# Optimization experiments

Hardware: AMD Instinct MI355X
Metric: run time of the kernel (lower is better)

## Reference

```python
import jax, jax.numpy as jnp
import numpy as np

B, S, H, F, E, N, K = 2, 4096, 1024, 3584, 8, 2, 2


def setup_inputs() -> dict:
    key = jax.random.key(0)
    ks = jax.random.split(key, 6)
    scale_h = 1.0 / np.sqrt(H)
    scale_f = 1.0 / np.sqrt(F)
    return {
        "hidden_states": jax.random.normal(ks[0], (B, S, H), dtype=jnp.float32),
        "gate_w": jax.random.normal(ks[1], (E, H), dtype=jnp.float32) * scale_h,
        "gate2_w": jax.random.normal(ks[2], (N, H), dtype=jnp.float32) * scale_h,
        "w1": jax.random.normal(ks[3], (E, F, H), dtype=jnp.float32) * scale_h,
        "w2": jax.random.normal(ks[4], (E, H, F), dtype=jnp.float32) * scale_f,
        "w3": jax.random.normal(ks[5], (E, F, H), dtype=jnp.float32) * scale_h,
    }


def reference(hidden_states, gate_w, gate2_w, w1, w2, w3):
    b, s, h = hidden_states.shape
    x = hidden_states.reshape(-1, h)  # [T, H]

    # Router: real gate + null-expert gate, concatenated
    router_logits = jnp.concatenate([x @ gate_w.T, x @ gate2_w.T], axis=1)  # [T, E+N]
    rw = jax.nn.softmax(router_logits.astype(jnp.float32), axis=1)
    top_w, sel = jax.lax.top_k(rw, K)  # [T, K]

    # Null experts (idx >= E) get their raw weight; real experts are renormalized
    mask = sel < E
    sw = top_w * mask
    denom = sw.sum(axis=-1, keepdims=True)
    denom = jnp.where(denom == 0, 1.0, denom)
    weights = (sw / denom + top_w * (~mask)).astype(x.dtype)  # [T, K]

    # Per-(token, real-expert) combine weight; null experts drop out (one_hot -> 0)
    combine = jnp.einsum("tke,tk->et", jax.nn.one_hot(sel, E, dtype=x.dtype), weights)  # [E, T]

    def body(acc, p):
        w1e, w2e, w3e, cw = p
        hgate = jax.nn.silu(x @ w1e.T) * (x @ w3e.T)  # [T, F]
        return acc + cw[:, None] * (hgate @ w2e.T), None

    out, _ = jax.lax.scan(body, jnp.zeros_like(x), (w1, w2, w3, combine))
    return out.reshape(b, s, h), router_logits
```

## Files before the change

### kernel.cpp

```cpp
#include <hip/hip_runtime.h>
#include <hip/hip_bf16.h>

namespace {

constexpr int T_TOK = 8192;
constexpr int HDIM  = 1024;
constexpr int FDIM  = 3584;
constexpr int CAP_ROWS = 17408;
constexpr int MAXMT = CAP_ROWS / 128;

typedef __bf16 bf16x8 __attribute__((ext_vector_type(8)));
typedef float  f32x4  __attribute__((ext_vector_type(4)));

__device__ inline unsigned short f2bf(float f) {
  union { float f; unsigned u; } a; a.f = f;
  unsigned r = a.u + 0x7fffu + ((a.u >> 16) & 1u);
  return (unsigned short)(r >> 16);
}

typedef const __attribute__((address_space(1))) void* gptr_t;
typedef __attribute__((address_space(3))) void* lptr_t;
__device__ inline void gload_lds16(const void* g, void* l) {
  __builtin_amdgcn_global_load_lds((gptr_t)g, (lptr_t)l, 16, 0, 0);
}

__global__ void k_init(int* meta) {
  if (threadIdx.x < 32) meta[threadIdx.x] = 0;
}

__global__ __launch_bounds__(256) void k_router(
    const float* __restrict__ x, const float* __restrict__ gw,
    const float* __restrict__ gw2, float* __restrict__ logits_out,
    int* __restrict__ sel, float* __restrict__ wts)
{
  int t = blockIdx.x * 4 + (threadIdx.x >> 6);
  int lane = threadIdx.x & 63;
  if (t >= T_TOK) return;
  const float* xr = x + (size_t)t * HDIM;
  float acc[10];
#pragma unroll
  for (int e = 0; e < 10; ++e) acc[e] = 0.f;
#pragma unroll
  for (int it = 0; it < 4; ++it) {
    int base = it * 256 + lane * 4;
    float4 xv = *reinterpret_cast<const float4*>(xr + base);
#pragma unroll
    for (int e = 0; e < 8; ++e) {
      float4 g = *reinterpret_cast<const float4*>(gw + e * HDIM + base);
      acc[e] += xv.x * g.x + xv.y * g.y + xv.z * g.z + xv.w * g.w;
    }
#pragma unroll
    for (int e = 0; e < 2; ++e) {
      float4 g = *reinterpret_cast<const float4*>(gw2 + e * HDIM + base);
      acc[8 + e] += xv.x * g.x + xv.y * g.y + xv.z * g.z + xv.w * g.w;
    }
  }
#pragma unroll
  for (int e = 0; e < 10; ++e) {
#pragma unroll
    for (int off = 32; off > 0; off >>= 1)
      acc[e] += __shfl_xor(acc[e], off, 64);
  }
  if (lane == 0) {
    float* lo = logits_out + (size_t)t * 10;
#pragma unroll
    for (int e = 0; e < 10; ++e) lo[e] = acc[e];
    float mx = acc[0];
#pragma unroll
    for (int e = 1; e < 10; ++e) mx = fmaxf(mx, acc[e]);
    float p[10], s = 0.f;
#pragma unroll
    for (int e = 0; e < 10; ++e) { p[e] = __expf(acc[e] - mx); s += p[e]; }
    float inv = 1.f / s;
#pragma unroll
    for (int e = 0; e < 10; ++e) p[e] *= inv;
    int i0 = 0;
    for (int e = 1; e < 10; ++e) if (p[e] > p[i0]) i0 = e;
    int i1 = (i0 == 0) ? 1 : 0;
    for (int e = 0; e < 10; ++e) if (e != i0 && p[e] > p[i1]) i1 = e;
    float w0 = p[i0], w1 = p[i1];
    bool r0 = i0 < 8, r1 = i1 < 8;
    float den = (r0 ? w0 : 0.f) + (r1 ? w1 : 0.f);
    if (den == 0.f) den = 1.f;
    sel[t * 2]     = i0; wts[t * 2]     = r0 ? w0 / den : 0.f;
    sel[t * 2 + 1] = i1; wts[t * 2 + 1] = r1 ? w1 / den : 0.f;
  }
}

__global__ __launch_bounds__(256) void k_hist(
    const int* __restrict__ sel, int* __restrict__ meta)
{
  __shared__ int part[256][8];
  int tid = threadIdx.x;
  int c[8];
#pragma unroll
  for (int e = 0; e < 8; ++e) c[e] = 0;
  for (int i = 0; i < 64; ++i) {
    int v = sel[i * 256 + tid];
#pragma unroll
    for (int e = 0; e < 8; ++e) c[e] += (v == e);
  }
#pragma unroll
  for (int e = 0; e < 8; ++e) part[tid][e] = c[e];
  __syncthreads();
  for (int s = 128; s >= 1; s >>= 1) {
    if (tid < s) {
#pragma unroll
      for (int e = 0; e < 8; ++e) part[tid][e] += part[tid + s][e];
    }
    __syncthreads();
  }
  if (tid < 8) meta[tid] = part[0][tid];
}

__global__ void k_seg(int* meta) {
  if (threadIdx.x != 0 || blockIdx.x != 0) return;
  int off = 0;
  for (int e = 0; e < 8; ++e) {
    meta[16 + e] = off;
    int c = meta[e];
    int pad = (c + 127) & ~127;
    int t0 = off >> 7, nt = pad >> 7;
    for (int i = 0; i < nt; ++i) meta[32 + t0 + i] = e;
    off += pad;
    meta[8 + e] = 0;
  }
  meta[24] = off;
  meta[25] = off >> 7;
}

__global__ __launch_bounds__(256) void k_zeropad(
    const int* __restrict__ meta, unsigned short* __restrict__ xg)
{
  int e = blockIdx.x >> 7, r = blockIdx.x & 127;
  int c = meta[e];
  int pad = (c + 127) & ~127;
  if (c + r >= pad) return;
  size_t row = (size_t)meta[16 + e] + c + r;
  reinterpret_cast<ushort4*>(xg + row * HDIM)[threadIdx.x] = ushort4{0, 0, 0, 0};
}

__global__ __launch_bounds__(256) void k_scatter(
    const float* __restrict__ x, const int* __restrict__ sel,
    int* __restrict__ meta, int* __restrict__ pair_row,
    unsigned short* __restrict__ xg)
{
  __shared__ int s_cnt[8];
  __shared__ int s_base[8];
  __shared__ int s_row[256];
  int tid = threadIdx.x;
  int pair0 = blockIdx.x * 256;
  if (tid < 8) s_cnt[tid] = 0;
  __syncthreads();
  int e = sel[pair0 + tid];
  int rank = -1;
  if (e < 8) rank = atomicAdd(&s_cnt[e], 1);
  __syncthreads();
  if (tid < 8) {
    int c = s_cnt[tid];
    s_base[tid] = c > 0 ? atomicAdd(&meta[8 + tid], c) : 0;
  }
  __syncthreads();
  int row = (e < 8) ? meta[16 + e] + s_base[e] + rank : -1;
  pair_row[pair0 + tid] = row;
  s_row[tid] = row;
  __syncthreads();
  int wid = tid >> 6, lane = tid & 63;
  for (int i = wid; i < 256; i += 4) {
    int r = s_row[i];
    if (r < 0) continue;
    const float* xr = x + (size_t)((pair0 + i) >> 1) * HDIM;
    unsigned short* dst = xg + (size_t)r * HDIM;
#pragma unroll
    for (int it = 0; it < 4; ++it) {
      int base = it * 256 + lane * 4;
      float4 v = *reinterpret_cast<const float4*>(xr + base);
      ushort4 o{f2bf(v.x), f2bf(v.y), f2bf(v.z), f2bf(v.w)};
      *reinterpret_cast<ushort4*>(dst + base) = o;
    }
  }
}

__global__ __launch_bounds__(256) void k_conv(
    const float* __restrict__ src, unsigned short* __restrict__ dst,
    long long nrows, long long rowlen, long long sstride)
{
  long long i = ((long long)blockIdx.x * 256 + threadIdx.x) * 8;
  if (i >= nrows * rowlen) return;
  long long r = i / rowlen, c = i - r * rowlen;
  const float4* s = reinterpret_cast<const float4*>(src + r * sstride + c);
  float4 a = s[0], b = s[1];
  ushort4* d = reinterpret_cast<ushort4*>(dst + i);
  d[0] = ushort4{f2bf(a.x), f2bf(a.y), f2bf(a.z), f2bf(a.w)};
  d[1] = ushort4{f2bf(b.x), f2bf(b.y), f2bf(b.z), f2bf(b.w)};
}

__global__ __launch_bounds__(256) void k_gemm1(
    const unsigned short* __restrict__ xg,
    const unsigned short* __restrict__ wc1,
    const unsigned short* __restrict__ wc3,
    unsigned short* __restrict__ hg,
    const int* __restrict__ meta, int Fc)
{
  __shared__ unsigned short As[128 * 32];
  __shared__ unsigned short B1s[64 * 32];
  __shared__ unsigned short B3s[64 * 32];

  int mt = blockIdx.y;
  if (mt >= meta[25]) return;
  int e = meta[32 + mt];
  int mrow0 = mt * 128;
  int fl0 = blockIdx.x * 64;

  int tid = threadIdx.x, wid = tid >> 6, lane = tid & 63;
  int lr = lane & 15, lg = lane >> 4;
  int wm = wid >> 1, wn = wid & 1;

  f32x4 acc1[4][2], acc3[4][2];
  const f32x4 zero = {0.f, 0.f, 0.f, 0.f};
#pragma unroll
  for (int m = 0; m < 4; ++m)
#pragma unroll
    for (int n = 0; n < 2; ++n) { acc1[m][n] = zero; acc3[m][n] = zero; }

  const unsigned short* w1p = wc1 + ((size_t)e * Fc + fl0) * HDIM;
  const unsigned short* w3p = wc3 + ((size_t)e * Fc + fl0) * HDIM;

  int arow = tid >> 2, aco = (tid & 3) * 8;
  int brow = tid >> 2, bco = (tid & 3) * 8;

  for (int k0 = 0; k0 < HDIM; k0 += 32) {
#pragma unroll
    for (int i = 0; i < 2; ++i) {
      int slot = i * 256 + tid;
      gload_lds16(xg + (size_t)(mrow0 + (slot >> 2)) * HDIM + k0 + (slot & 3) * 8,
                  (char*)As + i * 4096 + wid * 1024);
    }
    gload_lds16(w1p + (size_t)brow * HDIM + k0 + bco, (char*)B1s + wid * 1024);
    gload_lds16(w3p + (size_t)brow * HDIM + k0 + bco, (char*)B3s + wid * 1024);
    __syncthreads();

    bf16x8 a[4], b1[2], b3[2];
#pragma unroll
    for (int m = 0; m < 4; ++m)
      a[m] = *reinterpret_cast<const bf16x8*>(&As[(wm * 64 + m * 16 + lr) * 32 + lg * 8]);
#pragma unroll
    for (int n = 0; n < 2; ++n) {
      b1[n] = *reinterpret_cast<const bf16x8*>(&B1s[(wn * 32 + n * 16 + lr) * 32 + lg * 8]);
      b3[n] = *reinterpret_cast<const bf16x8*>(&B3s[(wn * 32 + n * 16 + lr) * 32 + lg * 8]);
    }
#pragma unroll
    for (int m = 0; m < 4; ++m)
#pragma unroll
      for (int n = 0; n < 2; ++n) {
        acc1[m][n] = __builtin_amdgcn_mfma_f32_16x16x32_bf16(a[m], b1[n], acc1[m][n], 0, 0, 0);
        acc3[m][n] = __builtin_amdgcn_mfma_f32_16x16x32_bf16(a[m], b3[n], acc3[m][n], 0, 0, 0);
      }
    __syncthreads();
  }

#pragma unroll
  for (int m = 0; m < 4; ++m)
#pragma unroll
    for (int n = 0; n < 2; ++n) {
      int gcol = fl0 + wn * 32 + n * 16 + lr;
#pragma unroll
      for (int j = 0; j < 4; ++j) {
        int grow = mrow0 + wm * 64 + m * 16 + lg * 4 + j;
        float s1 = acc1[m][n][j];
        float s3 = acc3[m][n][j];
        float h = s1 / (1.f + __expf(-s1)) * s3;
        hg[(size_t)grow * Fc + gcol] = f2bf(h);
      }
    }
}

__global__ __launch_bounds__(256) void k_gemm2(
    const unsigned short* __restrict__ hg,
    const unsigned short* __restrict__ wc2,
    float* __restrict__ yrows, const int* __restrict__ meta,
    int Fc, int first)
{
  __shared__ unsigned short As[128 * 32];
  __shared__ unsigned short Bs[128 * 32];

  int mt = blockIdx.y;
  if (mt >= meta[25]) return;
  int e = meta[32 + mt];
  int mrow0 = mt * 128;
  int hcol0 = blockIdx.x * 128;

  int tid = threadIdx.x, wid = tid >> 6, lane = tid & 63;
  int lr = lane & 15, lg = lane >> 4;
  int wm = wid >> 1, wn = wid & 1;

  f32x4 acc[4][4];
  const f32x4 zero = {0.f, 0.f, 0.f, 0.f};
#pragma unroll
  for (int m = 0; m < 4; ++m)
#pragma unroll
    for (int n = 0; n < 4; ++n) acc[m][n] = zero;

  const unsigned short* w2p = wc2 + ((size_t)e * HDIM + hcol0) * Fc;

  for (int k0 = 0; k0 < Fc; k0 += 32) {
#pragma unroll
    for (int i = 0; i < 2; ++i) {
      int slot = i * 256 + tid;
      int row = slot >> 2, co = (slot & 3) * 8;
      gload_lds16(hg + (size_t)(mrow0 + row) * Fc + k0 + co,
                  (char*)As + i * 4096 + wid * 1024);
      gload_lds16(w2p + (size_t)row * Fc + k0 + co,
                  (char*)Bs + i * 4096 + wid * 1024);
    }
    __syncthreads();

    bf16x8 a[4], b[4];
#pragma unroll
    for (int m = 0; m < 4; ++m)
      a[m] = *reinterpret_cast<const bf16x8*>(&As[(wm * 64 + m * 16 + lr) * 32 + lg * 8]);
#pragma unroll
    for (int n = 0; n < 4; ++n)
      b[n] = *reinterpret_cast<const bf16x8*>(&Bs[(wn * 64 + n * 16 + lr) * 32 + lg * 8]);
#pragma unroll
    for (int m = 0; m < 4; ++m)
#pragma unroll
      for (int n = 0; n < 4; ++n)
        acc[m][n] = __builtin_amdgcn_mfma_f32_16x16x32_bf16(a[m], b[n], acc[m][n], 0, 0, 0);
    __syncthreads();
  }

#pragma unroll
  for (int m = 0; m < 4; ++m)
#pragma unroll
    for (int n = 0; n < 4; ++n) {
      int gcol = hcol0 + wn * 64 + n * 16 + lr;
#pragma unroll
      for (int j = 0; j < 4; ++j) {
        int grow = mrow0 + wm * 64 + m * 16 + lg * 4 + j;
        float* yp = yrows + (size_t)grow * HDIM + gcol;
        float v = acc[m][n][j];
        if (first) *yp = v; else *yp += v;
      }
    }
}

__global__ __launch_bounds__(256) void k_combine(
    const float* __restrict__ yrows, const int* __restrict__ pair_row,
    const float* __restrict__ wts, float* __restrict__ out)
{
  int t = blockIdx.x * 4 + (threadIdx.x >> 6);
  int lane = threadIdx.x & 63;
  if (t >= T_TOK) return;
  int r0 = pair_row[t * 2], r1 = pair_row[t * 2 + 1];
  float w0 = (r0 >= 0) ? wts[t * 2] : 0.f;
  float w1 = (r1 >= 0) ? wts[t * 2 + 1] : 0.f;
  const float* y0 = yrows + (size_t)(r0 >= 0 ? r0 : 0) * HDIM;
  const float* y1 = yrows + (size_t)(r1 >= 0 ? r1 : 0) * HDIM;
  float* op = out + (size_t)t * HDIM;
#pragma unroll
  for (int it = 0; it < 4; ++it) {
    int base = it * 256 + lane * 4;
    float4 a = *reinterpret_cast<const float4*>(y0 + base);
    float4 b = *reinterpret_cast<const float4*>(y1 + base);
    float4 r{w0 * a.x + w1 * b.x, w0 * a.y + w1 * b.y,
             w0 * a.z + w1 * b.z, w0 * a.w + w1 * b.w};
    *reinterpret_cast<float4*>(op + base) = r;
  }
}

}

extern "C" void kernel_launch(void* const* d_in, const int* in_sizes, int n_in,
                              void* d_out, int out_size, void* d_ws, size_t ws_size,
                              hipStream_t stream)
{
  const float* x   = (const float*)d_in[0];
  const float* gw  = (const float*)d_in[1];
  const float* gw2 = (const float*)d_in[2];
  const float* w1  = (const float*)d_in[3];
  const float* w2  = (const float*)d_in[4];
  const float* w3  = (const float*)d_in[5];
  float* out = (float*)d_out;
  float* logits_out = out + (size_t)T_TOK * HDIM;

  char* p = (char*)d_ws;
  int* meta = (int*)p;            p += 1024;
  int* sel = (int*)p;             p += T_TOK * 2 * sizeof(int);
  float* wts = (float*)p;         p += T_TOK * 2 * sizeof(float);
  int* pair_row = (int*)p;        p += T_TOK * 2 * sizeof(int);
  unsigned short* xg = (unsigned short*)p;  p += (size_t)CAP_ROWS * HDIM * 2;
  float* yrows = (float*)p;                 p += (size_t)CAP_ROWS * HDIM * 4;
  size_t fixed = (size_t)(p - (char*)d_ws);

  int nf = 28;
  const int opts[6] = {1, 2, 4, 7, 14, 28};
  for (int i = 0; i < 6; ++i) {
    size_t Fc_i = FDIM / opts[i];
    size_t need = fixed + 3 * 16384 * Fc_i + (size_t)CAP_ROWS * Fc_i * 2;
    if (need <= ws_size) { nf = opts[i]; break; }
  }
  int Fc = FDIM / nf;

  unsigned short* wc1 = (unsigned short*)p;  p += (size_t)16384 * Fc;
  unsigned short* wc3 = (unsigned short*)p;  p += (size_t)16384 * Fc;
  unsigned short* wc2 = (unsigned short*)p;  p += (size_t)16384 * Fc;
  unsigned short* hg  = (unsigned short*)p;

  k_init<<<1, 64, 0, stream>>>(meta);
  k_router<<<T_TOK / 4, 256, 0, stream>>>(x, gw, gw2, logits_out, sel, wts);
  k_hist<<<1, 256, 0, stream>>>(sel, meta);
  k_seg<<<1, 64, 0, stream>>>(meta);
  k_zeropad<<<1024, 256, 0, stream>>>(meta, xg);
  k_scatter<<<T_TOK * 2 / 256, 256, 0, stream>>>(x, sel, meta, pair_row, xg);

  for (int c = 0; c < nf; ++c) {
    long long c0 = (long long)c * Fc;
    long long rl13 = (long long)Fc * HDIM;
    int nb13 = (int)((8 * rl13 / 8 + 255) / 256);
    k_conv<<<nb13, 256, 0, stream>>>(w1 + c0 * HDIM, wc1, 8, rl13, (long long)FDIM * HDIM);
    k_conv<<<nb13, 256, 0, stream>>>(w3 + c0 * HDIM, wc3, 8, rl13, (long long)FDIM * HDIM);
    int nb2 = (int)(((long long)8 * HDIM * Fc / 8 + 255) / 256);
    k_conv<<<nb2, 256, 0, stream>>>(w2 + c0, wc2, 8 * HDIM, Fc, (long long)FDIM);

    k_gemm1<<<dim3(Fc / 64, MAXMT), 256, 0, stream>>>(xg, wc1, wc3, hg, meta, Fc);
    k_gemm2<<<dim3(HDIM / 128, MAXMT), 256, 0, stream>>>(hg, wc2, yrows, meta, Fc, c == 0 ? 1 : 0);
  }
  k_combine<<<T_TOK / 4, 256, 0, stream>>>(yrows, pair_row, wts, out);
}
```

Before: 631.0 us.

## Double GEMM K-tile with XOR-swizzled LDS, fuse weight conversions and routing metadata kernels

Both expert GEMMs now stage a 64-wide K slice per iteration instead of 32, which halves the barrier count and cuts loop overhead. The LDS layout uses an XOR swizzle on 16-byte chunks to avoid bank conflicts when reading MFMA fragments. The three weight-conversion launches per F-chunk are merged into one 3D-grid kernel with a fast path for contiguous rows. The init, histogram and segment kernels are fused into one, with tile-to-expert mapping done in parallel. The larger tiles double LDS use per block, which may reduce occupancy.

```diff
diff --git a/kernel.cpp b/kernel.cpp
--- a/kernel.cpp
+++ b/kernel.cpp
@@ -22,10 +22,6 @@
 typedef __attribute__((address_space(3))) void* lptr_t;
 __device__ inline void gload_lds16(const void* g, void* l) {
   __builtin_amdgcn_global_load_lds((gptr_t)g, (lptr_t)l, 16, 0, 0);
-}
-
-__global__ void k_init(int* meta) {
-  if (threadIdx.x < 32) meta[threadIdx.x] = 0;
 }
 
 __global__ __launch_bounds__(256) void k_router(
@@ -87,10 +83,11 @@
   }
 }
 
-__global__ __launch_bounds__(256) void k_hist(
+__global__ __launch_bounds__(256) void k_histseg(
     const int* __restrict__ sel, int* __restrict__ meta)
 {
   __shared__ int part[256][8];
+  __shared__ int s_tile0[9];
   int tid = threadIdx.x;
   int c[8];
 #pragma unroll
@@ -110,23 +107,27 @@
     }
     __syncthreads();
   }
-  if (tid < 8) meta[tid] = part[0][tid];
-}
-
-__global__ void k_seg(int* meta) {
-  if (threadIdx.x != 0 || blockIdx.x != 0) return;
-  int off = 0;
-  for (int e = 0; e < 8; ++e) {
-    meta[16 + e] = off;
-    int c = meta[e];
-    int pad = (c + 127) & ~127;
-    int t0 = off >> 7, nt = pad >> 7;
-    for (int i = 0; i < nt; ++i) meta[32 + t0 + i] = e;
-    off += pad;
-    meta[8 + e] = 0;
-  }
-  meta[24] = off;
-  meta[25] = off >> 7;
+  if (tid == 0) {
+    int off = 0;
+    for (int e = 0; e < 8; ++e) {
+      int cnt = part[0][e];
+      meta[e] = cnt;
+      meta[8 + e] = 0;
+      meta[16 + e] = off;
+      s_tile0[e] = off >> 7;
+      off += (cnt + 127) & ~127;
+    }
+    meta[24] = off;
+    meta[25] = off >> 7;
+    s_tile0[8] = off >> 7;
+  }
+  __syncthreads();
+  int nt = s_tile0[8];
+  if (tid < nt) {
+    int e = 0;
+    while (s_tile0[e + 1] <= tid) ++e;
+    meta[32 + tid] = e;
+  }
 }
 
 __global__ __launch_bounds__(256) void k_zeropad(
@@ -181,15 +182,29 @@
   }
 }
 
-__global__ __launch_bounds__(256) void k_conv(
-    const float* __restrict__ src, unsigned short* __restrict__ dst,
-    long long nrows, long long rowlen, long long sstride)
+__global__ __launch_bounds__(256) void k_conv3(
+    const float* __restrict__ s1, const float* __restrict__ s3,
+    const float* __restrict__ s2,
+    unsigned short* __restrict__ d1, unsigned short* __restrict__ d3,
+    unsigned short* __restrict__ d2,
+    long long total, long long rl13, long long ss13,
+    long long rl2, long long ss2)
 {
   long long i = ((long long)blockIdx.x * 256 + threadIdx.x) * 8;
-  if (i >= nrows * rowlen) return;
-  long long r = i / rowlen, c = i - r * rowlen;
-  const float4* s = reinterpret_cast<const float4*>(src + r * sstride + c);
-  float4 a = s[0], b = s[1];
+  if (i >= total) return;
+  const float* src; unsigned short* dst; long long rowlen, sstride;
+  if (blockIdx.y == 0)      { src = s1; dst = d1; rowlen = rl13; sstride = ss13; }
+  else if (blockIdx.y == 1) { src = s3; dst = d3; rowlen = rl13; sstride = ss13; }
+  else                      { src = s2; dst = d2; rowlen = rl2;  sstride = ss2;  }
+  const float* sp;
+  if (rowlen == sstride) {
+    sp = src + i;
+  } else {
+    long long r = i / rowlen, c = i - r * rowlen;
+    sp = src + r * sstride + c;
+  }
+  float4 a = reinterpret_cast<const float4*>(sp)[0];
+  float4 b = reinterpret_cast<const float4*>(sp)[1];
   ushort4* d = reinterpret_cast<ushort4*>(dst + i);
   d[0] = ushort4{f2bf(a.x), f2bf(a.y), f2bf(a.z), f2bf(a.w)};
   d[1] = ushort4{f2bf(b.x), f2bf(b.y), f2bf(b.z), f2bf(b.w)};
@@ -202,9 +217,9 @@
     unsigned short* __restrict__ hg,
     const int* __restrict__ meta, int Fc)
 {
-  __shared__ unsigned short As[128 * 32];
-  __shared__ unsigned short B1s[64 * 32];
-  __shared__ unsigned short B3s[64 * 32];
+  __shared__ unsigned short As[128 * 64];
+  __shared__ unsigned short B1s[64 * 64];
+  __shared__ unsigned short B3s[64 * 64];
 
   int mt = blockIdx.y;
   if (mt >= meta[25]) return;
@@ -226,36 +241,52 @@
   const unsigned short* w1p = wc1 + ((size_t)e * Fc + fl0) * HDIM;
   const unsigned short* w3p = wc3 + ((size_t)e * Fc + fl0) * HDIM;
 
-  int arow = tid >> 2, aco = (tid & 3) * 8;
-  int brow = tid >> 2, bco = (tid & 3) * 8;
-
-  for (int k0 = 0; k0 < HDIM; k0 += 32) {
+  int srow = tid >> 3;
+  int sc8  = tid & 7;
+
+  for (int k0 = 0; k0 < HDIM; k0 += 64) {
+#pragma unroll
+    for (int i = 0; i < 4; ++i) {
+      int row = i * 32 + srow;
+      int c8 = sc8 ^ (row & 7);
+      gload_lds16(xg + (size_t)(mrow0 + row) * HDIM + k0 + c8 * 8,
+                  (char*)As + i * 4096 + wid * 1024);
+    }
 #pragma unroll
     for (int i = 0; i < 2; ++i) {
-      int slot = i * 256 + tid;
-      gload_lds16(xg + (size_t)(mrow0 + (slot >> 2)) * HDIM + k0 + (slot & 3) * 8,
-                  (char*)As + i * 4096 + wid * 1024);
-    }
-    gload_lds16(w1p + (size_t)brow * HDIM + k0 + bco, (char*)B1s + wid * 1024);
-    gload_lds16(w3p + (size_t)brow * HDIM + k0 + bco, (char*)B3s + wid * 1024);
+      int row = i * 32 + srow;
+      int c8 = sc8 ^ (row & 7);
+      gload_lds16(w1p + (size_t)row * HDIM + k0 + c8 * 8,
+                  (char*)B1s + i * 4096 + wid * 1024);
+      gload_lds16(w3p + (size_t)row * HDIM + k0 + c8 * 8,
+                  (char*)B3s + i * 4096 + wid * 1024);
+    }
     __syncthreads();
 
-    bf16x8 a[4], b1[2], b3[2];
-#pragma unroll
-    for (int m = 0; m < 4; ++m)
-      a[m] = *reinterpret_cast<const bf16x8*>(&As[(wm * 64 + m * 16 + lr) * 32 + lg * 8]);
-#pragma unroll
-    for (int n = 0; n < 2; ++n) {
-      b1[n] = *reinterpret_cast<const bf16x8*>(&B1s[(wn * 32 + n * 16 + lr) * 32 + lg * 8]);
-      b3[n] = *reinterpret_cast<const bf16x8*>(&B3s[(wn * 32 + n * 16 + lr) * 32 + lg * 8]);
-    }
-#pragma unroll
-    for (int m = 0; m < 4; ++m)
+#pragma unroll
+    for (int kk = 0; kk < 2; ++kk) {
+      bf16x8 a[4], b1[2], b3[2];
+#pragma unroll
+      for (int m = 0; m < 4; ++m) {
+        int r = wm * 64 + m * 16 + lr;
+        int off = r * 128 + ((kk * 64 + lg * 16) ^ ((r & 7) << 4));
+        a[m] = *reinterpret_cast<const bf16x8*>((const char*)As + off);
+      }
 #pragma unroll
       for (int n = 0; n < 2; ++n) {
-        acc1[m][n] = __builtin_amdgcn_mfma_f32_16x16x32_bf16(a[m], b1[n], acc1[m][n], 0, 0, 0);
-        acc3[m][n] = __builtin_amdgcn_mfma_f32_16x16x32_bf16(a[m], b3[n], acc3[m][n], 0, 0, 0);
-      }
+        int r = wn * 32 + n * 16 + lr;
+        int off = r * 128 + ((kk * 64 + lg * 16) ^ ((r & 7) << 4));
+        b1[n] = *reinterpret_cast<const bf16x8*>((const char*)B1s + off);
+        b3[n] = *reinterpret_cast<const bf16x8*>((const char*)B3s + off);
+      }
+#pragma unroll
+      for (int m = 0; m < 4; ++m)
+#pragma unroll
+        for (int n = 0; n < 2; ++n) {
+          acc1[m][n] = __builtin_amdgcn_mfma_f32_16x16x32_bf16(a[m], b1[n], acc1[m][n], 0, 0, 0);
+          acc3[m][n] = __builtin_amdgcn_mfma_f32_16x16x32_bf16(a[m], b3[n], acc3[m][n], 0, 0, 0);
+        }
+    }
     __syncthreads();
   }
 
@@ -281,8 +312,8 @@
     float* __restrict__ yrows, const int* __restrict__ meta,
     int Fc, int first)
 {
-  __shared__ unsigned short As[128 * 32];
-  __shared__ unsigned short Bs[128 * 32];
+  __shared__ unsigned short As[128 * 64];
+  __shared__ unsigned short Bs[128 * 64];
 
   int mt = blockIdx.y;
   if (mt >= meta[25]) return;
@@ -303,30 +334,42 @@
 
   const unsigned short* w2p = wc2 + ((size_t)e * HDIM + hcol0) * Fc;
 
-  for (int k0 = 0; k0 < Fc; k0 += 32) {
-#pragma unroll
-    for (int i = 0; i < 2; ++i) {
-      int slot = i * 256 + tid;
-      int row = slot >> 2, co = (slot & 3) * 8;
-      gload_lds16(hg + (size_t)(mrow0 + row) * Fc + k0 + co,
+  int srow = tid >> 3;
+  int sc8  = tid & 7;
+
+  for (int k0 = 0; k0 < Fc; k0 += 64) {
+#pragma unroll
+    for (int i = 0; i < 4; ++i) {
+      int row = i * 32 + srow;
+      int c8 = sc8 ^ (row & 7);
+      gload_lds16(hg + (size_t)(mrow0 + row) * Fc + k0 + c8 * 8,
                   (char*)As + i * 4096 + wid * 1024);
-      gload_lds16(w2p + (size_t)row * Fc + k0 + co,
+      gload_lds16(w2p + (size_t)row * Fc + k0 + c8 * 8,
                   (char*)Bs + i * 4096 + wid * 1024);
     }
     __syncthreads();
 
-    bf16x8 a[4], b[4];
-#pragma unroll
-    for (int m = 0; m < 4; ++m)
-      a[m] = *reinterpret_cast<const bf16x8*>(&As[(wm * 64 + m * 16 + lr) * 32 + lg * 8]);
-#pragma unroll
-    for (int n = 0; n < 4; ++n)
-      b[n] = *reinterpret_cast<const bf16x8*>(&Bs[(wn * 64 + n * 16 + lr) * 32 + lg * 8]);
-#pragma unroll
-    for (int m = 0; m < 4; ++m)
-#pragma unroll
-      for (int n = 0; n < 4; ++n)
-        acc[m][n] = __builtin_amdgcn_mfma_f32_16x16x32_bf16(a[m], b[n], acc[m][n], 0, 0, 0);
+#pragma unroll
+    for (int kk = 0; kk < 2; ++kk) {
+      bf16x8 a[4], b[4];
+#pragma unroll
+      for (int m = 0; m < 4; ++m) {
+        int r = wm * 64 + m * 16 + lr;
+        int off = r * 128 + ((kk * 64 + lg * 16) ^ ((r & 7) << 4));
+        a[m] = *reinterpret_cast<const bf16x8*>((const char*)As + off);
+      }
+#pragma unroll
+      for (int n = 0; n < 4; ++n) {
+        int r = wn * 64 + n * 16 + lr;
+        int off = r * 128 + ((kk * 64 + lg * 16) ^ ((r & 7) << 4));
+        b[n] = *reinterpret_cast<const bf16x8*>((const char*)Bs + off);
+      }
+#pragma unroll
+      for (int m = 0; m < 4; ++m)
+#pragma unroll
+        for (int n = 0; n < 4; ++n)
+          acc[m][n] = __builtin_amdgcn_mfma_f32_16x16x32_bf16(a[m], b[n], acc[m][n], 0, 0, 0);
+    }
     __syncthreads();
   }
 
@@ -407,21 +450,19 @@
   unsigned short* wc2 = (unsigned short*)p;  p += (size_t)16384 * Fc;
   unsigned short* hg  = (unsigned short*)p;
 
-  k_init<<<1, 64, 0, stream>>>(meta);
   k_router<<<T_TOK / 4, 256, 0, stream>>>(x, gw, gw2, logits_out, sel, wts);
-  k_hist<<<1, 256, 0, stream>>>(sel, meta);
-  k_seg<<<1, 64, 0, stream>>>(meta);
+  k_histseg<<<1, 256, 0, stream>>>(sel, meta);
   k_zeropad<<<1024, 256, 0, stream>>>(meta, xg);
   k_scatter<<<T_TOK * 2 / 256, 256, 0, stream>>>(x, sel, meta, pair_row, xg);
 
+  long long total = 8LL * Fc * HDIM;
+  int ncb = (int)(total / 8 / 256);
   for (int c = 0; c < nf; ++c) {
     long long c0 = (long long)c * Fc;
-    long long rl13 = (long long)Fc * HDIM;
-    int nb13 = (int)((8 * rl13 / 8 + 255) / 256);
-    k_conv<<<nb13, 256, 0, stream>>>(w1 + c0 * HDIM, wc1, 8, rl13, (long long)FDIM * HDIM);
-    k_conv<<<nb13, 256, 0, stream>>>(w3 + c0 * HDIM, wc3, 8, rl13, (long long)FDIM * HDIM);
-    int nb2 = (int)(((long long)8 * HDIM * Fc / 8 + 255) / 256);
-    k_conv<<<nb2, 256, 0, stream>>>(w2 + c0, wc2, 8 * HDIM, Fc, (long long)FDIM);
+    k_conv3<<<dim3(ncb, 3), 256, 0, stream>>>(
+        w1 + c0 * HDIM, w3 + c0 * HDIM, w2 + c0, wc1, wc3, wc2,
+        total, (long long)Fc * HDIM, (long long)FDIM * HDIM,
+        (long long)Fc, (long long)FDIM);
 
     k_gemm1<<<dim3(Fc / 64, MAXMT), 256, 0, stream>>>(xg, wc1, wc3, hg, meta, Fc);
     k_gemm2<<<dim3(HDIM / 128, MAXMT), 256, 0, stream>>>(hg, wc2, yrows, meta, Fc, c == 0 ? 1 : 0);
```

After: 561.2 us. -11.1%, faster.
